# Optimization experiments

Hardware: AMD Instinct MI355X
Metric: run time of the kernel (lower is better)

The kernel has to match this reference:

```python
import jax, jax.numpy as jnp
import numpy as np


def conv1x1(x, w, b):
    # x: (B, C_in, D, H, W), w: (C_out, C_in), b: (C_out,)  -- 1x1x1 Conv3d == per-voxel linear
    return jnp.einsum('bcdhw,oc->bodhw', x, w) + b[None, :, None, None, None]


def setup_inputs() -> dict:
    key = jax.random.key(0)
    ks = jax.random.split(key, 6)
    B, C, D, H, W = 2, 64, 8, 64, 64
    K = 4096  # codebook_size after halving
    return {
        'z': jax.random.normal(ks[0], (B, C, D, H, W), dtype=jnp.float32),
        'embedding': jax.random.normal(ks[1], (K, C), dtype=jnp.float32),
        'pre_w': jax.random.normal(ks[2], (C, C), dtype=jnp.float32) * (1.0 / np.sqrt(C)),
        'pre_b': jax.random.normal(ks[3], (C,), dtype=jnp.float32) * 0.01,
        'post_w': jax.random.normal(ks[4], (C, C), dtype=jnp.float32) * (1.0 / np.sqrt(C)),
        'post_b': jax.random.normal(ks[5], (C,), dtype=jnp.float32) * 0.01,
    }


def reference(z, embedding, pre_w, pre_b, post_w, post_b):
    B, C, D, H, W = z.shape
    x = conv1x1(z, pre_w, pre_b)  # pre_quant_conv

    # ---- quantize() ----
    # tokens: (B*D*H*W, C)
    t = jnp.transpose(x, (0, 2, 3, 4, 1)).reshape(-1, C)
    # squared euclidean distances (argmin identical to torch.cdist argmin)
    dist2 = (jnp.sum(t * t, axis=-1, keepdims=True)
             - 2.0 * t @ embedding.T
             + jnp.sum(embedding * embedding, axis=-1)[None, :])  # (N, K)
    idx = jnp.argmin(dist2, axis=-1)  # (N,)
    q = embedding[idx]  # gather: (N, C)

    commitment_loss = jnp.mean((jax.lax.stop_gradient(q) - t) ** 2)
    codebook_loss = jnp.mean((q - jax.lax.stop_gradient(t)) ** 2)

    # straight-through estimator
    q = t + jax.lax.stop_gradient(q - t)
    quant = jnp.transpose(q.reshape(B, D, H, W, C), (0, 4, 1, 2, 3))

    out = conv1x1(quant, post_w, post_b)  # post_quant_conv
    indices = idx.reshape(B, D, H, W)
    return out, codebook_loss, commitment_loss, indices
```

## Files before the change

### kernel.cpp

```cpp
#include <hip/hip_runtime.h>
#include <cstdint>
#include <cstddef>

typedef float  f32x4  __attribute__((ext_vector_type(4)));
typedef float  f32x16 __attribute__((ext_vector_type(16)));
typedef short  s16x8  __attribute__((ext_vector_type(8)));

#define DEV __device__ __forceinline__

static constexpr int    DHW       = 32768;
static constexpr int    NTOK      = 65536;
static constexpr int    CHUNK_B   = 18432;
static constexpr size_t OUT_ELEMS = 4194304;
static constexpr float  BIGC      = 512.0f;
static constexpr float  TAU       = 0.015f;
static constexpr int    FLAG_CAP  = 7424;

static constexpr size_t WS_PREP = 0;
static constexpr size_t WS_RESW = 1179648;
static constexpr size_t WS_RESB = 2228224;
static constexpr size_t WS_PART = 2490368;
static constexpr size_t WS_CNT  = 2494464;
static constexpr size_t WS_FLAG = 2494720;

DEV unsigned f2bf(float f) {
  unsigned u = __float_as_uint(f);
  return (u + 0x7FFFu + ((u >> 16) & 1u)) >> 16;
}
DEV float bf2f(unsigned h) { return __uint_as_float(h << 16); }
DEV unsigned med3u(unsigned a, unsigned b, unsigned c) {
  unsigned r;
  asm("v_med3_u32 %0, %1, %2, %3" : "=v"(r) : "v"(a), "v"(b), "v"(c));
  return r;
}
DEV void gl_lds16(const void* g, void* l) {
  __builtin_amdgcn_global_load_lds(
      (const __attribute__((address_space(1))) unsigned int*)g,
      (__attribute__((address_space(3))) unsigned int*)l, 16, 0, 0);
}

__global__ __launch_bounds__(256) void k_pre(const float* __restrict__ z,
    const float* __restrict__ emb, const float* __restrict__ pw, const float* __restrict__ pb,
    float* __restrict__ dout, char* __restrict__ ws)
{
  const int blk = blockIdx.x, tid = threadIdx.x;
  if (blk == 0 && tid == 0) *(int*)(ws + WS_CNT) = 0;
  if (blk < 1024) {
    float* t = dout;
    const int v = (blk & 255) * 256 + tid;
    const int qtr = blk >> 8;
    const int b = v >> 15, r = v & (DHW - 1);
    const float* zp = z + (size_t)b * 64 * DHW + r;
    float zr[64];
#pragma unroll
    for (int c2 = 0; c2 < 64; ++c2) zr[c2] = zp[(size_t)c2 * DHW];
    const int c0 = qtr * 16;
    for (int c = c0; c < c0 + 16; c += 4) {
      const float* w0 = pw + c * 64;
      const float* w1 = pw + (c + 1) * 64;
      const float* w2 = pw + (c + 2) * 64;
      const float* w3 = pw + (c + 3) * 64;
      float a0 = pb[c], a1 = pb[c + 1], a2 = pb[c + 2], a3 = pb[c + 3];
#pragma unroll
      for (int c2 = 0; c2 < 64; ++c2) {
        const float zv = zr[c2];
        a0 = fmaf(w0[c2], zv, a0); a1 = fmaf(w1[c2], zv, a1);
        a2 = fmaf(w2[c2], zv, a2); a3 = fmaf(w3[c2], zv, a3);
      }
      t[(size_t)c * NTOK + v]       = a0;
      t[(size_t)(c + 1) * NTOK + v] = a1;
      t[(size_t)(c + 2) * NTOK + v] = a2;
      t[(size_t)(c + 3) * NTOK + v] = a3;
    }
  } else {
    const int tt = (blk - 1024) * 256 + tid;
#pragma unroll
    for (int uu = 0; uu < 2; ++uu) {
      const int u = tt * 2 + uu;
      const int k = u >> 3, j = u & 7;
      const float* ep = emb + (size_t)k * 64 + j * 8;
      unsigned hw[4], lw[4];
#pragma unroll
      for (int i = 0; i < 4; ++i) {
        float g0 = -2.0f * ep[2 * i], g1 = -2.0f * ep[2 * i + 1];
        unsigned h0 = f2bf(g0); unsigned l0 = f2bf(g0 - bf2f(h0));
        unsigned h1 = f2bf(g1); unsigned l1 = f2bf(g1 - bf2f(h1));
        hw[i] = h0 | (h1 << 16); lw[i] = l0 | (l1 << 16);
      }
      char* base = ws + WS_PREP + (size_t)(k >> 6) * CHUNK_B;
      const int r = k & 63;
      const int swz = (r & 15) << 4;
      char* rowp = base + r * 256;
      *(uint4*)(rowp + ((j * 16) ^ swz))        = make_uint4(hw[0], hw[1], hw[2], hw[3]);
      *(uint4*)(rowp + ((128 + j * 16) ^ swz))  = make_uint4(lw[0], lw[1], lw[2], lw[3]);
      if (j == 0) {
        const float* er = emb + (size_t)k * 64;
        float s = 0.f;
#pragma unroll
        for (int c = 0; c < 64; ++c) s = fmaf(er[c], er[c], s);
        s += BIGC;
        unsigned eh  = f2bf(s);
        float    rs  = s - bf2f(eh);
        unsigned el  = f2bf(rs);
        unsigned el2 = f2bf(rs - bf2f(el));
        *(uint4*)(base + 16384 + r * 16) = make_uint4(eh | (el << 16), el2, 0u, 0u);
        if (r == 0) *(uint4*)(base + 16384 + 1024) = make_uint4(0u, 0u, 0u, 0u);
      }
    }
  }
}

__global__ __launch_bounds__(1024, 4) void k_dist(float* __restrict__ dout,
                                                  char* __restrict__ ws)
{
  constexpr int NCH = 16;
  __shared__ __align__(16) char smem[2 * CHUNK_B];
  __shared__ float t2s[16];
  const float* t = dout;
  const int tid = threadIdx.x;
  const int w = tid >> 6, lane = tid & 63;
  const int l31 = lane & 31, khalf = lane >> 5;
  const int gidx = blockIdx.x >> 2, h = blockIdx.x & 3;
  const int tb = gidx * 512 + w * 32;
  const int tok = tb + l31;

  s16x8 tav[4], tlv[4];
  float t2 = 0.f;
#pragma unroll
  for (int kt = 0; kt < 4; ++kt) {
    const float* tc = t + (size_t)(kt * 16 + khalf * 8) * NTOK + tok;
    float f[8];
#pragma unroll
    for (int i = 0; i < 8; ++i) f[i] = tc[(size_t)i * NTOK];
#pragma unroll
    for (int i = 0; i < 8; ++i) t2 = fmaf(f[i], f[i], t2);
    union { unsigned u[4]; s16x8 v; } xh, xl;
#pragma unroll
    for (int i = 0; i < 4; ++i) {
      unsigned h0 = f2bf(f[2 * i]),     l0 = f2bf(f[2 * i]     - bf2f(h0));
      unsigned h1 = f2bf(f[2 * i + 1]), l1 = f2bf(f[2 * i + 1] - bf2f(h1));
      xh.u[i] = h0 | (h1 << 16); xl.u[i] = l0 | (l1 << 16);
    }
    tav[kt] = xh.v; tlv[kt] = xl.v;
  }
  t2 += __shfl_xor(t2, 32);
#pragma unroll
  for (int m = 1; m <= 16; m <<= 1) t2 += __shfl_xor(t2, m);
  if (lane == 0) t2s[w] = t2;

  s16x8 ones;
  { union { unsigned u[4]; s16x8 v; } o;
    o.u[0] = khalf ? 0u : 0x3F803F80u;
    o.u[1] = khalf ? 0u : 0x00003F80u;
    o.u[2] = 0u; o.u[3] = 0u; ones = o.v; }

  const char* prep = ws + WS_PREP + (size_t)h * NCH * CHUNK_B;
  const int swz = (l31 & 15) << 4;

  auto stage = [&](int cc) {
    const char* src = prep + (size_t)cc * CHUNK_B;
    char* dst = smem + (size_t)(cc & 1) * CHUNK_B;
    gl_lds16(src + w * 1024 + lane * 16, dst + w * 1024);
    if (w < 2) gl_lds16(src + 16384 + w * 1024 + lane * 16, dst + 16384 + w * 1024);
  };
  stage(0);
  __syncthreads();

  unsigned u1 = 0x7f800000u, u2 = 0x7f800000u;
  int c1 = 0;

  for (int c = 0; c < NCH; ++c) {
    const char* L = smem + (c & 1) * CHUNK_B;
    if (c + 1 < NCH) stage(c + 1);
    f32x16 acc0 = {}, acc1 = {};
    {
      const s16x8 e0 = *(const s16x8*)(L + (khalf ? (16384 + 1024) : (16384 + l31 * 16)));
      const s16x8 e1 = *(const s16x8*)(L + (khalf ? (16384 + 1024) : (16384 + (32 + l31) * 16)));
      acc0 = __builtin_amdgcn_mfma_f32_32x32x16_bf16(e0, ones, acc0, 0, 0, 0);
      acc1 = __builtin_amdgcn_mfma_f32_32x32x16_bf16(e1, ones, acc1, 0, 0, 0);
    }
#pragma unroll
    for (int kt = 0; kt < 4; ++kt) {
      const int i0 = (kt * 32 + khalf * 16) ^ swz;
      const s16x8 gh0 = *(const s16x8*)(L + l31 * 256 + i0);
      const s16x8 gl0 = *(const s16x8*)(L + l31 * 256 + (i0 ^ 128));
      const s16x8 gh1 = *(const s16x8*)(L + (32 + l31) * 256 + i0);
      const s16x8 gl1 = *(const s16x8*)(L + (32 + l31) * 256 + (i0 ^ 128));
      acc0 = __builtin_amdgcn_mfma_f32_32x32x16_bf16(gh0, tav[kt], acc0, 0, 0, 0);
      acc0 = __builtin_amdgcn_mfma_f32_32x32x16_bf16(gh0, tlv[kt], acc0, 0, 0, 0);
      acc0 = __builtin_amdgcn_mfma_f32_32x32x16_bf16(gl0, tav[kt], acc0, 0, 0, 0);
      acc1 = __builtin_amdgcn_mfma_f32_32x32x16_bf16(gh1, tav[kt], acc1, 0, 0, 0);
      acc1 = __builtin_amdgcn_mfma_f32_32x32x16_bf16(gh1, tlv[kt], acc1, 0, 0, 0);
      acc1 = __builtin_amdgcn_mfma_f32_32x32x16_bf16(gl1, tav[kt], acc1, 0, 0, 0);
    }
    const unsigned p1 = u1;
#pragma unroll
    for (int q = 0; q < 16; ++q) {
      const unsigned w0 = (unsigned)((q & 3) + 8 * (q >> 2));
      unsigned v0 = (__float_as_uint(acc0[q]) & ~63u) | w0;
      u2 = med3u(u1, v0, u2); u1 = u1 < v0 ? u1 : v0;
      unsigned v1 = (__float_as_uint(acc1[q]) & ~63u) | (w0 + 32u);
      u2 = med3u(u1, v1, u2); u1 = u1 < v1 ? u1 : v1;
    }
    if (u1 != p1) c1 = c;
    __syncthreads();
  }

  u1 |= (unsigned)(khalf * 4);
  const unsigned o1 = __shfl_xor(u1, 32);
  const unsigned o2 = __shfl_xor(u2, 32);
  const int      oc = __shfl_xor(c1, 32);
  const unsigned am = u1 & ~63u, om = o1 & ~63u;
  const int mycode = c1 * 64 + (int)(u1 & 63u);
  const int ocode  = oc * 64 + (int)(o1 & 63u);
  const bool owins = (om < am) || (om == am && ocode < mycode);
  const unsigned f1 = owins ? o1 : u1;
  const int      fc = owins ? oc : c1;
  const unsigned mx = owins ? am : om;
  unsigned s2 = (u2 & ~63u) < (o2 & ~63u) ? (u2 & ~63u) : (o2 & ~63u);
  s2 = s2 < mx ? s2 : mx;
  if (khalf == 0) {
    const bool nt = (__uint_as_float(s2) - __uint_as_float(f1 & ~63u)) < TAU;
    ((unsigned*)(ws + WS_RESW))[h * 65536 + tok] = f1;
    ((unsigned char*)(ws + WS_RESB))[h * 65536 + tok] =
        (unsigned char)(fc | (nt ? 0x80 : 0));
  }
  if (h == 0 && tid == 0) {
    float s = 0.f;
#pragma unroll
    for (int i = 0; i < 16; ++i) s += t2s[i];
    ((float*)(ws + WS_PART))[256 + gidx] = s;
  }
}

__global__ __launch_bounds__(256) void k_merge(float* __restrict__ dout,
                                               char* __restrict__ ws)
{
  __shared__ float ls[4];
  const int tid = threadIdx.x;
  const int v = blockIdx.x * 256 + tid;
  const unsigned* resw = (const unsigned*)(ws + WS_RESW);
  const unsigned char* resb = (const unsigned char*)(ws + WS_RESB);
  unsigned k1 = 0xffffffffu, k2 = 0xffffffffu, bw = 0; int bq = 0;
#pragma unroll
  for (int q = 0; q < 4; ++q) {
    const unsigned W = resw[q * 65536 + v];
    const unsigned key = W & ~63u;
    if (key < k1) { k2 = k1; k1 = key; bq = q; bw = W; }
    else          { k2 = key < k2 ? key : k2; }
  }
  const unsigned char bb = resb[bq * 65536 + v];
  const int code = bq * 1024 + (int)(bb & 15u) * 64 + (int)(bw & 63u);
  dout[OUT_ELEMS + 2 + v] = (float)code;
  const bool flag = (bb & 0x80u) ||
                    (__uint_as_float(k2) - __uint_as_float(k1) < TAU);
  if (flag) {
    int p = atomicAdd((int*)(ws + WS_CNT), 1);
    if (p < FLAG_CAP) ((int*)(ws + WS_FLAG))[p] = v;
  }
  float acc = __uint_as_float(k1) - 512.0f;
#pragma unroll
  for (int m = 1; m <= 32; m <<= 1) acc += __shfl_xor(acc, m);
  const int lane = tid & 63, wv = tid >> 6;
  if (lane == 0) ls[wv] = acc;
  __syncthreads();
  if (tid == 0)
    ((float*)(ws + WS_PART))[blockIdx.x] = ls[0] + ls[1] + ls[2] + ls[3];
}

__global__ __launch_bounds__(256) void k_refine(const float* __restrict__ z,
    const float* __restrict__ emb, const float* __restrict__ pw, const float* __restrict__ pb,
    float* __restrict__ dout, char* __restrict__ ws)
{
  __shared__ double tdsh[64];
  __shared__ double dred[4]; __shared__ int kred[4];
  int cv = *(const int*)(ws + WS_CNT);
  if (cv > FLAG_CAP) cv = FLAG_CAP;
  const int tid = threadIdx.x;
  const int lane = tid & 63, wv = tid >> 6;

  for (int slot = blockIdx.x; slot < cv; slot += 256) {
    const int n = ((const int*)(ws + WS_FLAG))[slot];

    if (tid < 64) {
      const int b = n >> 15, r = n & (DHW - 1);
      const float* zp = z + (size_t)b * 64 * DHW + r;
      const float* wr = pw + tid * 64;
      double a = (double)pb[tid];
      for (int c2 = 0; c2 < 64; ++c2)
        a = fma((double)wr[c2], (double)zp[(size_t)c2 * DHW], a);
      tdsh[tid] = a;
    }
    __syncthreads();

    double td[64];
#pragma unroll
    for (int j = 0; j < 64; ++j) td[j] = tdsh[j];

    double dmin = 1e300; int kmin = 0;
    for (int it = 0; it < 16; ++it) {
      const int code = it * 256 + tid;
      const float4* e = (const float4*)(emb + (size_t)code * 64);
      double d0 = 0.0, d1 = 0.0;
#pragma unroll
      for (int i = 0; i < 16; ++i) {
        const float4 ev = e[i];
        const double x0 = td[4 * i]     - (double)ev.x; d0 = fma(x0, x0, d0);
        const double x1 = td[4 * i + 1] - (double)ev.y; d1 = fma(x1, x1, d1);
        const double x2 = td[4 * i + 2] - (double)ev.z; d0 = fma(x2, x2, d0);
        const double x3 = td[4 * i + 3] - (double)ev.w; d1 = fma(x3, x3, d1);
      }
      const double d = d0 + d1;
      if (d < dmin) { dmin = d; kmin = code; }
    }
#pragma unroll
    for (int m = 1; m < 64; m <<= 1) {
      const double od = __shfl_xor(dmin, m);
      const int    ok = __shfl_xor(kmin, m);
      if (od < dmin || (od == dmin && ok < kmin)) { dmin = od; kmin = ok; }
    }
    if (lane == 0) { dred[wv] = dmin; kred[wv] = kmin; }
    __syncthreads();
    if (tid == 0) {
#pragma unroll
      for (int i = 1; i < 4; ++i)
        if (dred[i] < dmin || (dred[i] == dmin && kred[i] < kmin)) { dmin = dred[i]; kmin = kred[i]; }
      dout[OUT_ELEMS + 2 + n] = (float)kmin;
    }
    __syncthreads();
  }
}

__global__ __launch_bounds__(256) void k_post(const float* __restrict__ emb,
    const float* __restrict__ ow, const float* __restrict__ ob,
    float* __restrict__ dout, const char* __restrict__ ws)
{
  __shared__ float ps[256];
  const int v = (blockIdx.x & 255) * 256 + threadIdx.x;
  const int qtr = blockIdx.x >> 8;
  const int b = v >> 15, r = v & (DHW - 1);
  const int code = (int)dout[OUT_ELEMS + 2 + v];
  const float* q = emb + (size_t)code * 64;
  float qr[64];
#pragma unroll
  for (int i = 0; i < 16; ++i) *(float4*)(qr + i * 4) = *(const float4*)(q + i * 4);
  float* op = dout + (size_t)b * 64 * DHW + r;
  const int o0 = qtr * 16;
  for (int o = o0; o < o0 + 16; o += 4) {
    const float* w0 = ow + o * 64;
    const float* w1 = ow + (o + 1) * 64;
    const float* w2 = ow + (o + 2) * 64;
    const float* w3 = ow + (o + 3) * 64;
    float a0 = ob[o], a1 = ob[o + 1], a2 = ob[o + 2], a3 = ob[o + 3];
#pragma unroll
    for (int cch = 0; cch < 64; ++cch) {
      const float qv = qr[cch];
      a0 = fmaf(w0[cch], qv, a0); a1 = fmaf(w1[cch], qv, a1);
      a2 = fmaf(w2[cch], qv, a2); a3 = fmaf(w3[cch], qv, a3);
    }
    op[(size_t)o * DHW]       = a0;
    op[(size_t)(o + 1) * DHW] = a1;
    op[(size_t)(o + 2) * DHW] = a2;
    op[(size_t)(o + 3) * DHW] = a3;
  }
  if (blockIdx.x == 0) {
    const float* part = (const float*)(ws + WS_PART);
    const int t4 = threadIdx.x * 4;
    float s = 0.f;
    if (threadIdx.x < 96)
      s = ((part[t4] + part[t4 + 1]) + part[t4 + 2]) + part[t4 + 3];
    ps[threadIdx.x] = s;
    __syncthreads();
    if (threadIdx.x == 0) {
      float tot = 0.f;
      for (int i = 0; i < 256; ++i) tot += ps[i];
      const float mean = tot / 4194304.0f;
      dout[OUT_ELEMS]     = mean;
      dout[OUT_ELEMS + 1] = mean;
    }
  }
}

extern "C" void kernel_launch(void* const* d_in, const int* in_sizes, int n_in,
                              void* d_out, int out_size, void* d_ws, size_t ws_size,
                              hipStream_t stream) {
  (void)in_sizes; (void)n_in; (void)out_size; (void)ws_size;
  const float* z   = (const float*)d_in[0];
  const float* emb = (const float*)d_in[1];
  const float* pw  = (const float*)d_in[2];
  const float* pb  = (const float*)d_in[3];
  const float* ow  = (const float*)d_in[4];
  const float* ob  = (const float*)d_in[5];
  float* out = (float*)d_out;
  char*  ws  = (char*)d_ws;

  hipLaunchKernelGGL(k_pre,    dim3(1088), dim3(256),  0, stream, z, emb, pw, pb, out, ws);
  hipLaunchKernelGGL(k_dist,   dim3(512),  dim3(1024), 0, stream, out, ws);
  hipLaunchKernelGGL(k_merge,  dim3(256),  dim3(256),  0, stream, out, ws);
  hipLaunchKernelGGL(k_refine, dim3(256),  dim3(256),  0, stream, z, emb, pw, pb, out, ws);
  hipLaunchKernelGGL(k_post,   dim3(1024), dim3(256),  0, stream, emb, ow, ob, out, ws);
}
```

Baseline: 171.5 us.

## Fuse merge with post-conv, recompute refined tokens' output in refine kernel

Merges the argmin-merge kernel with the post-quant 1x1 conv, staging gathered codebook rows in LDS, so one launch and the round trip of codes through global memory disappear. The refine kernel now recomputes the post-conv output for the flagged tokens it corrects, and an extra block in it computes the loss reduction. The pre-conv kernel switches to 1024-thread blocks that load the z tile into LDS once via global_load_lds, so z is no longer re-read by four separate blocks. The cost is a heavier refine pass and higher LDS use per block, which may lower occupancy.

Result: slower. 215.4 us (+25.6%).

```diff
diff --git a/kernel.cpp b/kernel.cpp
--- a/kernel.cpp
+++ b/kernel.cpp
@@ -39,21 +39,30 @@
       (__attribute__((address_space(3))) unsigned int*)l, 16, 0, 0);
 }
 
-__global__ __launch_bounds__(256) void k_pre(const float* __restrict__ z,
+__global__ __launch_bounds__(1024) void k_pre(const float* __restrict__ z,
     const float* __restrict__ emb, const float* __restrict__ pw, const float* __restrict__ pb,
     float* __restrict__ dout, char* __restrict__ ws)
 {
+  __shared__ __align__(16) float zlds[64 * 256];
   const int blk = blockIdx.x, tid = threadIdx.x;
   if (blk == 0 && tid == 0) *(int*)(ws + WS_CNT) = 0;
-  if (blk < 1024) {
+  if (blk < 256) {
     float* t = dout;
-    const int v = (blk & 255) * 256 + tid;
-    const int qtr = blk >> 8;
-    const int b = v >> 15, r = v & (DHW - 1);
-    const float* zp = z + (size_t)b * 64 * DHW + r;
+    const int v0 = blk * 256;
+    const int b = v0 >> 15, r0 = v0 & (DHW - 1);
+    const int w = tid >> 6, lane = tid & 63;
+#pragma unroll
+    for (int k = 0; k < 4; ++k) {
+      const int c2 = w * 4 + k;
+      gl_lds16(z + (size_t)(b * 64 + c2) * DHW + r0 + lane * 4,
+               (char*)zlds + c2 * 1024);
+    }
+    __syncthreads();
+    const int i = tid & 255, qtr = tid >> 8;
+    const int v = v0 + i;
     float zr[64];
 #pragma unroll
-    for (int c2 = 0; c2 < 64; ++c2) zr[c2] = zp[(size_t)c2 * DHW];
+    for (int c2 = 0; c2 < 64; ++c2) zr[c2] = zlds[c2 * 256 + i];
     const int c0 = qtr * 16;
     for (int c = c0; c < c0 + 16; c += 4) {
       const float* w0 = pw + c * 64;
@@ -73,7 +82,7 @@
       t[(size_t)(c + 3) * NTOK + v] = a3;
     }
   } else {
-    const int tt = (blk - 1024) * 256 + tid;
+    const int tt = (blk - 256) * 1024 + tid;
 #pragma unroll
     for (int uu = 0; uu < 2; ++uu) {
       const int u = tt * 2 + uu;
@@ -233,57 +242,118 @@
   }
 }
 
-__global__ __launch_bounds__(256) void k_merge(float* __restrict__ dout,
-                                               char* __restrict__ ws)
+__global__ __launch_bounds__(1024) void k_postm(const float* __restrict__ emb,
+    const float* __restrict__ ow, const float* __restrict__ ob,
+    float* __restrict__ dout, char* __restrict__ ws)
 {
+  __shared__ float qlds[256 * 65];
+  __shared__ int   codes[256];
   __shared__ float ls[4];
-  const int tid = threadIdx.x;
-  const int v = blockIdx.x * 256 + tid;
-  const unsigned* resw = (const unsigned*)(ws + WS_RESW);
-  const unsigned char* resb = (const unsigned char*)(ws + WS_RESB);
-  unsigned k1 = 0xffffffffu, k2 = 0xffffffffu, bw = 0; int bq = 0;
-#pragma unroll
-  for (int q = 0; q < 4; ++q) {
-    const unsigned W = resw[q * 65536 + v];
-    const unsigned key = W & ~63u;
-    if (key < k1) { k2 = k1; k1 = key; bq = q; bw = W; }
-    else          { k2 = key < k2 ? key : k2; }
-  }
-  const unsigned char bb = resb[bq * 65536 + v];
-  const int code = bq * 1024 + (int)(bb & 15u) * 64 + (int)(bw & 63u);
-  dout[OUT_ELEMS + 2 + v] = (float)code;
-  const bool flag = (bb & 0x80u) ||
-                    (__uint_as_float(k2) - __uint_as_float(k1) < TAU);
-  if (flag) {
-    int p = atomicAdd((int*)(ws + WS_CNT), 1);
-    if (p < FLAG_CAP) ((int*)(ws + WS_FLAG))[p] = v;
-  }
-  float acc = __uint_as_float(k1) - 512.0f;
-#pragma unroll
-  for (int m = 1; m <= 32; m <<= 1) acc += __shfl_xor(acc, m);
-  const int lane = tid & 63, wv = tid >> 6;
-  if (lane == 0) ls[wv] = acc;
+  const int tid = threadIdx.x, blk = blockIdx.x;
+  if (tid < 256) {
+    const int v = blk * 256 + tid;
+    const unsigned* resw = (const unsigned*)(ws + WS_RESW);
+    const unsigned char* resb = (const unsigned char*)(ws + WS_RESB);
+    unsigned k1 = 0xffffffffu, k2 = 0xffffffffu, bw = 0; int bq = 0;
+#pragma unroll
+    for (int q = 0; q < 4; ++q) {
+      const unsigned W = resw[q * 65536 + v];
+      const unsigned key = W & ~63u;
+      if (key < k1) { k2 = k1; k1 = key; bq = q; bw = W; }
+      else          { k2 = key < k2 ? key : k2; }
+    }
+    const unsigned char bb = resb[bq * 65536 + v];
+    const int code = bq * 1024 + (int)(bb & 15u) * 64 + (int)(bw & 63u);
+    codes[tid] = code;
+    dout[OUT_ELEMS + 2 + v] = (float)code;
+    const bool flag = (bb & 0x80u) ||
+                      (__uint_as_float(k2) - __uint_as_float(k1) < TAU);
+    if (flag) {
+      int p = atomicAdd((int*)(ws + WS_CNT), 1);
+      if (p < FLAG_CAP) ((int*)(ws + WS_FLAG))[p] = v;
+    }
+    float acc = __uint_as_float(k1) - 512.0f;
+#pragma unroll
+    for (int m = 1; m <= 32; m <<= 1) acc += __shfl_xor(acc, m);
+    if ((tid & 63) == 0) ls[tid >> 6] = acc;
+  }
   __syncthreads();
   if (tid == 0)
-    ((float*)(ws + WS_PART))[blockIdx.x] = ls[0] + ls[1] + ls[2] + ls[3];
+    ((float*)(ws + WS_PART))[blk] = ls[0] + ls[1] + ls[2] + ls[3];
+  {
+    const int ti = tid >> 2, p = tid & 3;
+    const float* src = emb + (size_t)codes[ti] * 64 + p * 16;
+    float* drow = qlds + ti * 65 + p * 16;
+#pragma unroll
+    for (int j = 0; j < 4; ++j) {
+      const float4 qv = *(const float4*)(src + j * 4);
+      drow[j * 4]     = qv.x; drow[j * 4 + 1] = qv.y;
+      drow[j * 4 + 2] = qv.z; drow[j * 4 + 3] = qv.w;
+    }
+  }
+  __syncthreads();
+  const int i = tid & 255, qtr = tid >> 8;
+  const int v = blk * 256 + i;
+  const int b = v >> 15, r = v & (DHW - 1);
+  float qr[64];
+#pragma unroll
+  for (int cch = 0; cch < 64; ++cch) qr[cch] = qlds[i * 65 + cch];
+  float* op = dout + (size_t)b * 64 * DHW + r;
+  const int o0 = qtr * 16;
+  for (int o = o0; o < o0 + 16; o += 4) {
+    const float* w0 = ow + o * 64;
+    const float* w1 = ow + (o + 1) * 64;
+    const float* w2 = ow + (o + 2) * 64;
+    const float* w3 = ow + (o + 3) * 64;
+    float a0 = ob[o], a1 = ob[o + 1], a2 = ob[o + 2], a3 = ob[o + 3];
+#pragma unroll
+    for (int cch = 0; cch < 64; ++cch) {
+      const float qv = qr[cch];
+      a0 = fmaf(w0[cch], qv, a0); a1 = fmaf(w1[cch], qv, a1);
+      a2 = fmaf(w2[cch], qv, a2); a3 = fmaf(w3[cch], qv, a3);
+    }
+    op[(size_t)o * DHW]       = a0;
+    op[(size_t)(o + 1) * DHW] = a1;
+    op[(size_t)(o + 2) * DHW] = a2;
+    op[(size_t)(o + 3) * DHW] = a3;
+  }
 }
 
 __global__ __launch_bounds__(256) void k_refine(const float* __restrict__ z,
     const float* __restrict__ emb, const float* __restrict__ pw, const float* __restrict__ pb,
+    const float* __restrict__ ow, const float* __restrict__ ob,
     float* __restrict__ dout, char* __restrict__ ws)
 {
   __shared__ double tdsh[64];
   __shared__ double dred[4]; __shared__ int kred[4];
+  __shared__ int kwin;
+  const int tid = threadIdx.x;
+  if (blockIdx.x == 256) {
+    __shared__ float ps[256];
+    const float* part = (const float*)(ws + WS_PART);
+    const int t4 = tid * 4;
+    float s = 0.f;
+    if (tid < 96) s = ((part[t4] + part[t4 + 1]) + part[t4 + 2]) + part[t4 + 3];
+    ps[tid] = s;
+    __syncthreads();
+    if (tid == 0) {
+      float tot = 0.f;
+      for (int i = 0; i < 256; ++i) tot += ps[i];
+      const float mean = tot / 4194304.0f;
+      dout[OUT_ELEMS]     = mean;
+      dout[OUT_ELEMS + 1] = mean;
+    }
+    return;
+  }
   int cv = *(const int*)(ws + WS_CNT);
   if (cv > FLAG_CAP) cv = FLAG_CAP;
-  const int tid = threadIdx.x;
   const int lane = tid & 63, wv = tid >> 6;
 
   for (int slot = blockIdx.x; slot < cv; slot += 256) {
     const int n = ((const int*)(ws + WS_FLAG))[slot];
+    const int b = n >> 15, r = n & (DHW - 1);
 
     if (tid < 64) {
-      const int b = n >> 15, r = n & (DHW - 1);
       const float* zp = z + (size_t)b * 64 * DHW + r;
       const float* wr = pw + tid * 64;
       double a = (double)pb[tid];
@@ -326,58 +396,18 @@
       for (int i = 1; i < 4; ++i)
         if (dred[i] < dmin || (dred[i] == dmin && kred[i] < kmin)) { dmin = dred[i]; kmin = kred[i]; }
       dout[OUT_ELEMS + 2 + n] = (float)kmin;
-    }
-    __syncthreads();
-  }
-}
-
-__global__ __launch_bounds__(256) void k_post(const float* __restrict__ emb,
-    const float* __restrict__ ow, const float* __restrict__ ob,
-    float* __restrict__ dout, const char* __restrict__ ws)
-{
-  __shared__ float ps[256];
-  const int v = (blockIdx.x & 255) * 256 + threadIdx.x;
-  const int qtr = blockIdx.x >> 8;
-  const int b = v >> 15, r = v & (DHW - 1);
-  const int code = (int)dout[OUT_ELEMS + 2 + v];
-  const float* q = emb + (size_t)code * 64;
-  float qr[64];
-#pragma unroll
-  for (int i = 0; i < 16; ++i) *(float4*)(qr + i * 4) = *(const float4*)(q + i * 4);
-  float* op = dout + (size_t)b * 64 * DHW + r;
-  const int o0 = qtr * 16;
-  for (int o = o0; o < o0 + 16; o += 4) {
-    const float* w0 = ow + o * 64;
-    const float* w1 = ow + (o + 1) * 64;
-    const float* w2 = ow + (o + 2) * 64;
-    const float* w3 = ow + (o + 3) * 64;
-    float a0 = ob[o], a1 = ob[o + 1], a2 = ob[o + 2], a3 = ob[o + 3];
-#pragma unroll
-    for (int cch = 0; cch < 64; ++cch) {
-      const float qv = qr[cch];
-      a0 = fmaf(w0[cch], qv, a0); a1 = fmaf(w1[cch], qv, a1);
-      a2 = fmaf(w2[cch], qv, a2); a3 = fmaf(w3[cch], qv, a3);
-    }
-    op[(size_t)o * DHW]       = a0;
-    op[(size_t)(o + 1) * DHW] = a1;
-    op[(size_t)(o + 2) * DHW] = a2;
-    op[(size_t)(o + 3) * DHW] = a3;
-  }
-  if (blockIdx.x == 0) {
-    const float* part = (const float*)(ws + WS_PART);
-    const int t4 = threadIdx.x * 4;
-    float s = 0.f;
-    if (threadIdx.x < 96)
-      s = ((part[t4] + part[t4 + 1]) + part[t4 + 2]) + part[t4 + 3];
-    ps[threadIdx.x] = s;
-    __syncthreads();
-    if (threadIdx.x == 0) {
-      float tot = 0.f;
-      for (int i = 0; i < 256; ++i) tot += ps[i];
-      const float mean = tot / 4194304.0f;
-      dout[OUT_ELEMS]     = mean;
-      dout[OUT_ELEMS + 1] = mean;
-    }
+      kwin = kmin;
+    }
+    __syncthreads();
+    if (tid < 64) {
+      const int o = tid;
+      const float* q = emb + (size_t)kwin * 64;
+      const float* wr = ow + o * 64;
+      float a = ob[o];
+      for (int cch = 0; cch < 64; ++cch) a = fmaf(wr[cch], q[cch], a);
+      dout[(size_t)b * 64 * DHW + (size_t)o * DHW + r] = a;
+    }
+    __syncthreads();
   }
 }
 
@@ -394,9 +424,8 @@
   float* out = (float*)d_out;
   char*  ws  = (char*)d_ws;
 
-  hipLaunchKernelGGL(k_pre,    dim3(1088), dim3(256),  0, stream, z, emb, pw, pb, out, ws);
-  hipLaunchKernelGGL(k_dist,   dim3(512),  dim3(1024), 0, stream, out, ws);
-  hipLaunchKernelGGL(k_merge,  dim3(256),  dim3(256),  0, stream, out, ws);
-  hipLaunchKernelGGL(k_refine, dim3(256),  dim3(256),  0, stream, z, emb, pw, pb, out, ws);
-  hipLaunchKernelGGL(k_post,   dim3(1024), dim3(256),  0, stream, emb, ow, ob, out, ws);
-}
+  hipLaunchKernelGGL(k_pre,    dim3(272), dim3(1024), 0, stream, z, emb, pw, pb, out, ws);
+  hipLaunchKernelGGL(k_dist,   dim3(512), dim3(1024), 0, stream, out, ws);
+  hipLaunchKernelGGL(k_postm,  dim3(256), dim3(1024), 0, stream, emb, ow, ob, out, ws);
+  hipLaunchKernelGGL(k_refine, dim3(257), dim3(256),  0, stream, z, emb, pw, pb, ow, ob, out, ws);
+}
```
